# Optimization experiments

Hardware: AMD Instinct MI355X
Metric: run time of the kernel (lower is better)

The kernel has to match this reference:

```python
import jax, jax.numpy as jnp
import numpy as np

N = 50000      # n_nodes
E = 800000     # edges (before self-loops)
IN = 128       # in_dim
HID = 32       # hidden_dim (per-head out channels)
HEADS = 4
EMB = 128      # embed_dim
LAYERS = 3
NEG_SLOPE = 0.2  # PyG GATv2 default leaky_relu slope


def _layer_norm(x, g, b):
    mu = jnp.mean(x, axis=-1, keepdims=True)
    var = jnp.var(x, axis=-1, keepdims=True)
    return g * (x - mu) / jnp.sqrt(var + 1e-5) + b


def _gatv2(h, src, dst, n, Wl, bl, Wr, br, att, bias):
    # GATv2Conv (PyG semantics, share_weights=False, concat=True).
    H, C = att.shape
    xl = (h @ Wl + bl).reshape(n, H, C)   # target (i) transform
    xr = (h @ Wr + br).reshape(n, H, C)   # source (j) transform
    x_i = xl[dst]                          # [Etot, H, C] gather
    x_j = xr[src]
    e = jax.nn.leaky_relu(x_i + x_j, NEG_SLOPE)
    logit = jnp.einsum('ehc,hc->eh', e, att)          # [Etot, H]
    # segment softmax over destination node (every node has a self-loop)
    m = jax.ops.segment_max(logit, dst, num_segments=n)
    ex = jnp.exp(logit - m[dst])
    den = jax.ops.segment_sum(ex, dst, num_segments=n)
    alpha = ex / (den[dst] + 1e-16)
    out = jax.ops.segment_sum(alpha[..., None] * x_j, dst, num_segments=n)
    return out.reshape(n, H * C) + bias


def setup_inputs() -> dict:
    key = jax.random.key(0)
    ks = iter(jax.random.split(key, 64))
    d = {}
    d['x'] = jax.random.normal(next(ks), (N, IN), jnp.float32)
    d['edge_index'] = jax.random.randint(next(ks), (2, E), 0, N, dtype=jnp.int64)

    def w(shape, fan):
        return jax.random.normal(next(ks), shape, jnp.float32) / np.float32(np.sqrt(fan))

    HC = HID * HEADS
    d['W_in'] = w((IN, HID), IN); d['b_in'] = jnp.zeros((HID,), jnp.float32)
    for i in range(LAYERS):
        ic = HID if i == 0 else HC
        d[f'Wl{i}'] = w((ic, HC), ic); d[f'bl{i}'] = jnp.zeros((HC,), jnp.float32)
        d[f'Wr{i}'] = w((ic, HC), ic); d[f'br{i}'] = jnp.zeros((HC,), jnp.float32)
        d[f'att{i}'] = w((HEADS, HID), HID)
        d[f'bo{i}'] = jnp.zeros((HC,), jnp.float32)
        d[f'g{i}'] = jnp.ones((HC,), jnp.float32)
        d[f'be{i}'] = jnp.zeros((HC,), jnp.float32)
    d['W_out'] = w((HC, EMB), HC); d['b_out'] = jnp.zeros((EMB,), jnp.float32)
    return d


def reference(x, edge_index, W_in, b_in,
              Wl0, bl0, Wr0, br0, att0, bo0, g0, be0,
              Wl1, bl1, Wr1, br1, att1, bo1, g1, be1,
              Wl2, bl2, Wr2, br2, att2, bo2, g2, be2,
              W_out, b_out):
    n = x.shape[0]
    loops = jnp.arange(n, dtype=edge_index.dtype)  # add_self_loops=True
    src = jnp.concatenate([edge_index[0], loops])
    dst = jnp.concatenate([edge_index[1], loops])

    h = jax.nn.gelu(x @ W_in + b_in, approximate=False)
    layers = [(Wl0, bl0, Wr0, br0, att0, bo0, g0, be0),
              (Wl1, bl1, Wr1, br1, att1, bo1, g1, be1),
              (Wl2, bl2, Wr2, br2, att2, bo2, g2, be2)]
    for (Wl, bl, Wr, br, att, bo, g, be) in layers:
        h_new = jax.nn.gelu(_layer_norm(_gatv2(h, src, dst, n, Wl, bl, Wr, br, att, bo), g, be), approximate=False)
        h = h + h_new if h.shape == h_new.shape else h_new  # dropout = identity (eval)
    out = h @ W_out + b_out
    norm = jnp.maximum(jnp.linalg.norm(out, axis=-1, keepdims=True), 1e-12)
    return out / norm
```

## Files before the change

### kernel.cpp

```cpp
#include <hip/hip_runtime.h>
#include <hip/hip_bf16.h>
#include <math.h>

#define N_NODES 50000
#define N_EDGES 800000
#define IN_DIM  128
#define HC_DIM  128
#define HID_C   32
#define SCAN_NB 196

typedef __attribute__((ext_vector_type(8))) short short8;
typedef __attribute__((ext_vector_type(4))) float f32x4;

__device__ __forceinline__ float gelu_f(float x){
    return 0.5f*x*(1.0f + erff(x*0.7071067811865475f));
}

__device__ __forceinline__ void split2(float f, short& h, short& l){
    __hip_bfloat16 bh = __float2bfloat16(f);
    float r = f - __bfloat162float(bh);
    __hip_bfloat16 blo = __float2bfloat16(r);
    h = *reinterpret_cast<short*>(&bh);
    l = *reinterpret_cast<short*>(&blo);
}

__global__ __launch_bounds__(256) void k_zero(int* __restrict__ p, int n){
    int i = blockIdx.x*256 + threadIdx.x;
    if(i<n) p[i]=0;
}

__global__ __launch_bounds__(256) void k_count(const int* __restrict__ dst, int* __restrict__ cnt){
    int e = blockIdx.x*256 + threadIdx.x;
    if(e<N_EDGES) atomicAdd(&cnt[dst[e]], 1);
}

__global__ __launch_bounds__(256) void k_scan1(const int* __restrict__ cnt, int* __restrict__ rowptr,
                                               int* __restrict__ part){
    __shared__ int sh[256];
    int t=threadIdx.x; int i=blockIdx.x*256+t;
    int v = (i<N_NODES)? cnt[i] : 0;
    sh[t]=v; __syncthreads();
    for(int off=1; off<256; off<<=1){
        int y = (t>=off)? sh[t-off] : 0;
        __syncthreads();
        sh[t] += y;
        __syncthreads();
    }
    if(i<N_NODES) rowptr[i] = sh[t]-v;
    if(t==255) part[blockIdx.x] = sh[255];
}

__global__ __launch_bounds__(256) void k_scan2(int* __restrict__ part){
    __shared__ int sh[256];
    int t=threadIdx.x;
    int v = (t<SCAN_NB)? part[t] : 0;
    sh[t]=v; __syncthreads();
    for(int off=1; off<256; off<<=1){
        int y=(t>=off)? sh[t-off]:0;
        __syncthreads();
        sh[t]+=y;
        __syncthreads();
    }
    if(t<SCAN_NB) part[t] = sh[t]-v;
}

__global__ __launch_bounds__(256) void k_scan3(int* __restrict__ rowptr, const int* __restrict__ part,
                                               int* __restrict__ cur){
    int t=threadIdx.x; int i=blockIdx.x*256+t;
    if(i<N_NODES){
        int v = rowptr[i] + part[blockIdx.x];
        rowptr[i]=v; cur[i]=v;
    }
    if(i==0) rowptr[N_NODES]=N_EDGES;
}

__global__ __launch_bounds__(256) void k_fill(const int* __restrict__ src, const int* __restrict__ dst,
                                              int* __restrict__ cur, int* __restrict__ col){
    int e = blockIdx.x*256+threadIdx.x;
    if(e<N_EDGES){
        int d = dst[e];
        int p = atomicAdd(&cur[d],1);
        col[p] = src[e];
    }
}

__global__ __launch_bounds__(256) void k_gemm_in(const float* __restrict__ x, const float* __restrict__ W,
                                                 const float* __restrict__ b, float* __restrict__ h){
    int id = blockIdx.x*256+threadIdx.x;
    int r = id>>5, c = id&31;
    const float4* x4 = (const float4*)(x + (size_t)r*IN_DIM);
    float acc=0.f;
    #pragma unroll 8
    for(int k=0;k<IN_DIM/4;k++){
        float4 xv = x4[k];
        acc = fmaf(xv.x, W[(4*k  )*HID_C+c], acc);
        acc = fmaf(xv.y, W[(4*k+1)*HID_C+c], acc);
        acc = fmaf(xv.z, W[(4*k+2)*HID_C+c], acc);
        acc = fmaf(xv.w, W[(4*k+3)*HID_C+c], acc);
    }
    h[r*HID_C+c] = gelu_f(acc + b[c]);
}

template<int K, bool PAIR>
__global__ __launch_bounds__(256) void k_mfma(const float* __restrict__ A,
                                              const float* __restrict__ Wl, const float* __restrict__ bl,
                                              const float* __restrict__ Wr, const float* __restrict__ br,
                                              float* __restrict__ XL, float* __restrict__ XR){
    constexpr int KC  = 32;
    constexpr int LDS_K = KC + 8;
    constexpr int NCH = K / KC;
    __shared__ short As_hi[64*LDS_K], As_lo[64*LDS_K];
    __shared__ short Wlh[64*LDS_K],  Wll[64*LDS_K];
    __shared__ short Wrh[64*LDS_K],  Wrl[64*LDS_K];

    int t = threadIdx.x;
    int lane = t & 63, wave = t >> 6;
    int quad = lane >> 4, ml = lane & 15;
    int rbase = blockIdx.x * 64;
    int nbase = blockIdx.y * 64;

    f32x4 accL[4], accR[4];
    #pragma unroll
    for(int i=0;i<4;i++){ accL[i] = (f32x4){0.f,0.f,0.f,0.f}; accR[i] = (f32x4){0.f,0.f,0.f,0.f}; }

    for(int c=0; c<NCH; c++){
        if(c) __syncthreads();
        {
            int r = t >> 2, seg = t & 3;
            int gr = rbase + r; if(gr >= N_NODES) gr = N_NODES-1;
            const float* src = A + (size_t)gr*K + c*KC + seg*8;
            float4 f0 = *(const float4*)src;
            float4 f1 = *(const float4*)(src+4);
            float fs[8] = {f0.x,f0.y,f0.z,f0.w,f1.x,f1.y,f1.z,f1.w};
            short8 vh, vl;
            #pragma unroll
            for(int j=0;j<8;j++){ short h,l; split2(fs[j],h,l); vh[j]=h; vl[j]=l; }
            *(short8*)(As_hi + r*LDS_K + seg*8) = vh;
            *(short8*)(As_lo + r*LDS_K + seg*8) = vl;
        }
        {
            int n = t & 63, kq = t >> 6;
            #pragma unroll
            for(int p=0;p<8;p++){
                int kl = kq + p*4;
                short h,l;
                split2(Wl[(size_t)(c*KC + kl)*HC_DIM + nbase + n], h, l);
                Wlh[n*LDS_K + kl] = h; Wll[n*LDS_K + kl] = l;
                if(PAIR){
                    split2(Wr[(size_t)(c*KC + kl)*HC_DIM + nbase + n], h, l);
                    Wrh[n*LDS_K + kl] = h; Wrl[n*LDS_K + kl] = l;
                }
            }
        }
        __syncthreads();
        int k0 = quad*8;
        short8 wlh = *(const short8*)(Wlh + (wave*16 + ml)*LDS_K + k0);
        short8 wll = *(const short8*)(Wll + (wave*16 + ml)*LDS_K + k0);
        short8 wrh, wrl;
        if(PAIR){
            wrh = *(const short8*)(Wrh + (wave*16 + ml)*LDS_K + k0);
            wrl = *(const short8*)(Wrl + (wave*16 + ml)*LDS_K + k0);
        }
        #pragma unroll
        for(int i=0;i<4;i++){
            short8 ah = *(const short8*)(As_hi + (16*i + ml)*LDS_K + k0);
            short8 al = *(const short8*)(As_lo + (16*i + ml)*LDS_K + k0);
            accL[i] = __builtin_amdgcn_mfma_f32_16x16x32_bf16(ah, wlh, accL[i], 0,0,0);
            accL[i] = __builtin_amdgcn_mfma_f32_16x16x32_bf16(ah, wll, accL[i], 0,0,0);
            accL[i] = __builtin_amdgcn_mfma_f32_16x16x32_bf16(al, wlh, accL[i], 0,0,0);
            if(PAIR){
                accR[i] = __builtin_amdgcn_mfma_f32_16x16x32_bf16(ah, wrh, accR[i], 0,0,0);
                accR[i] = __builtin_amdgcn_mfma_f32_16x16x32_bf16(ah, wrl, accR[i], 0,0,0);
                accR[i] = __builtin_amdgcn_mfma_f32_16x16x32_bf16(al, wrh, accR[i], 0,0,0);
            }
        }
    }

    int col = nbase + wave*16 + ml;
    float bL = bl[col];
    float bR = PAIR ? br[col] : 0.f;
    #pragma unroll
    for(int i=0;i<4;i++){
        int row0 = rbase + 16*i + quad*4;
        #pragma unroll
        for(int r=0;r<4;r++){
            int gr = row0 + r;
            if(gr < N_NODES){
                XL[(size_t)gr*HC_DIM + col] = accL[i][r] + bL;
                if(PAIR) XR[(size_t)gr*HC_DIM + col] = accR[i][r] + bR;
            }
        }
    }
}

__global__ __launch_bounds__(256) void k_rownorm(const float* __restrict__ tmp, float* __restrict__ out){
    int wave=threadIdx.x>>6, lane=threadIdx.x&63;
    int node = blockIdx.x*4+wave;
    float2 v = *(const float2*)(tmp + (size_t)node*HC_DIM + 2*lane);
    float ss = v.x*v.x + v.y*v.y;
    #pragma unroll
    for(int msk=1;msk<64;msk<<=1) ss += __shfl_xor(ss,msk);
    float inv = 1.0f / fmaxf(sqrtf(ss), 1e-12f);
    *(float2*)(out + (size_t)node*HC_DIM + 2*lane) = make_float2(v.x*inv, v.y*inv);
}

__global__ __launch_bounds__(256) void k_node(const float* __restrict__ XL, const float* __restrict__ XR,
    const int* __restrict__ rowptr, const int* __restrict__ colidx,
    const float* __restrict__ att, const float* __restrict__ bo,
    const float* __restrict__ gg, const float* __restrict__ be,
    const float* __restrict__ hold, float* __restrict__ hout)
{
    int wave=threadIdx.x>>6, lane=threadIdx.x&63;
    int node = blockIdx.x*4+wave;
    int cg = lane & 31, half = lane >> 5;
    int c4 = cg << 2;

    float4 xl = *(const float4*)(XL + (size_t)node*HC_DIM + c4);
    float4 av = *(const float4*)(att + c4);
    int beg = rowptr[node], end = rowptr[node+1];

    #define EDGE_LOGIT(xj, q) { \
        float u0 = xl.x + xj.x; u0 = (u0>0.f)?u0:0.2f*u0; \
        float u1 = xl.y + xj.y; u1 = (u1>0.f)?u1:0.2f*u1; \
        float u2 = xl.z + xj.z; u2 = (u2>0.f)?u2:0.2f*u2; \
        float u3 = xl.w + xj.w; u3 = (u3>0.f)?u3:0.2f*u3; \
        q = fmaf(u0,av.x, fmaf(u1,av.y, fmaf(u2,av.z, u3*av.w))); \
        q += __shfl_xor(q,1); q += __shfl_xor(q,2); q += __shfl_xor(q,4); }

    float4 xs = *(const float4*)(XR + (size_t)node*HC_DIM + c4);
    float qs; EDGE_LOGIT(xs, qs)
    float m, ls; float4 acc;
    if(half==0){ m = qs; ls = 1.f; acc = xs; }
    else       { m = -INFINITY; ls = 0.f; acc = make_float4(0.f,0.f,0.f,0.f); }

    int P = end - beg;
    int nb = P >> 3;
    int base = beg;
    for(int b=0; b<nb; b++, base += 8){
        int j0 = colidx[base     + half];
        int j1 = colidx[base + 2 + half];
        int j2 = colidx[base + 4 + half];
        int j3 = colidx[base + 6 + half];
        float4 x0 = *(const float4*)(XR + (size_t)j0*HC_DIM + c4);
        float4 x1 = *(const float4*)(XR + (size_t)j1*HC_DIM + c4);
        float4 x2 = *(const float4*)(XR + (size_t)j2*HC_DIM + c4);
        float4 x3 = *(const float4*)(XR + (size_t)j3*HC_DIM + c4);
        float q0,q1,q2,q3;
        EDGE_LOGIT(x0,q0) EDGE_LOGIT(x1,q1) EDGE_LOGIT(x2,q2) EDGE_LOGIT(x3,q3)
        float nm = fmaxf(m, fmaxf(fmaxf(q0,q1),fmaxf(q2,q3)));
        float sc = __expf(m-nm);
        float e0 = __expf(q0-nm), e1 = __expf(q1-nm);
        float e2 = __expf(q2-nm), e3 = __expf(q3-nm);
        ls = fmaf(ls, sc, (e0+e1)+(e2+e3));
        acc.x = fmaf(acc.x, sc, fmaf(e0,x0.x, fmaf(e1,x1.x, fmaf(e2,x2.x, e3*x3.x))));
        acc.y = fmaf(acc.y, sc, fmaf(e0,x0.y, fmaf(e1,x1.y, fmaf(e2,x2.y, e3*x3.y))));
        acc.z = fmaf(acc.z, sc, fmaf(e0,x0.z, fmaf(e1,x1.z, fmaf(e2,x2.z, e3*x3.z))));
        acc.w = fmaf(acc.w, sc, fmaf(e0,x0.w, fmaf(e1,x1.w, fmaf(e2,x2.w, e3*x3.w))));
        m = nm;
    }
    #pragma unroll
    for(int i=0;i<4;i++){
        int idx = base + 2*i + half;
        if(idx < end){
            int j = colidx[idx];
            float4 xj = *(const float4*)(XR + (size_t)j*HC_DIM + c4);
            float q; EDGE_LOGIT(xj, q)
            float nm = fmaxf(m, q);
            float sc = __expf(m-nm);
            float p  = __expf(q-nm);
            ls = fmaf(ls, sc, p);
            acc.x = fmaf(acc.x, sc, p*xj.x);
            acc.y = fmaf(acc.y, sc, p*xj.y);
            acc.z = fmaf(acc.z, sc, p*xj.z);
            acc.w = fmaf(acc.w, sc, p*xj.w);
            m = nm;
        }
    }
    #undef EDGE_LOGIT

    {
        float mo  = __shfl_xor(m, 32);
        float lso = __shfl_xor(ls, 32);
        float4 ao;
        ao.x = __shfl_xor(acc.x,32); ao.y = __shfl_xor(acc.y,32);
        ao.z = __shfl_xor(acc.z,32); ao.w = __shfl_xor(acc.w,32);
        float nm = fmaxf(m, mo);
        float s0 = __expf(m-nm), s1 = __expf(mo-nm);
        ls = ls*s0 + lso*s1;
        acc.x = acc.x*s0 + ao.x*s1;
        acc.y = acc.y*s0 + ao.y*s1;
        acc.z = acc.z*s0 + ao.z*s1;
        acc.w = acc.w*s0 + ao.w*s1;
    }

    float inv = 1.0f/ls;
    float4 bo4 = *(const float4*)(bo + c4);
    float o0 = fmaf(acc.x,inv,bo4.x), o1 = fmaf(acc.y,inv,bo4.y);
    float o2 = fmaf(acc.z,inv,bo4.z), o3 = fmaf(acc.w,inv,bo4.w);
    float s1v = (o0+o1)+(o2+o3);
    float s2v = fmaf(o0,o0, fmaf(o1,o1, fmaf(o2,o2, o3*o3)));
    #pragma unroll
    for(int msk=1;msk<32;msk<<=1){ s1v += __shfl_xor(s1v,msk); s2v += __shfl_xor(s2v,msk); }
    float mean = s1v*(1.f/128.f);
    float var  = s2v*(1.f/128.f) - mean*mean;
    float rstd = rsqrtf(var + 1e-5f);
    float4 g4  = *(const float4*)(gg + c4);
    float4 be4 = *(const float4*)(be + c4);
    float r0 = gelu_f(fmaf(g4.x*(o0-mean), rstd, be4.x));
    float r1 = gelu_f(fmaf(g4.y*(o1-mean), rstd, be4.y));
    float r2 = gelu_f(fmaf(g4.z*(o2-mean), rstd, be4.z));
    float r3 = gelu_f(fmaf(g4.w*(o3-mean), rstd, be4.w));
    if(hold){
        float4 hv = *(const float4*)(hold + (size_t)node*HC_DIM + c4);
        r0 += hv.x; r1 += hv.y; r2 += hv.z; r3 += hv.w;
    }
    if(half==0)
        *(float4*)(hout + (size_t)node*HC_DIM + c4) = make_float4(r0,r1,r2,r3);
}

extern "C" void kernel_launch(void* const* d_in, const int* in_sizes, int n_in,
                              void* d_out, int out_size, void* d_ws, size_t ws_size,
                              hipStream_t stream)
{
    const float* x   = (const float*)d_in[0];
    const int*   ei  = (const int*)  d_in[1];
    const float* Win = (const float*)d_in[2];
    const float* bin = (const float*)d_in[3];
    const float *Wl[3], *bl[3], *Wr[3], *br[3], *att[3], *bo[3], *gg[3], *be[3];
    for(int i=0;i<3;i++){
        const int base = 4 + 8*i;
        Wl[i]=(const float*)d_in[base+0]; bl[i]=(const float*)d_in[base+1];
        Wr[i]=(const float*)d_in[base+2]; br[i]=(const float*)d_in[base+3];
        att[i]=(const float*)d_in[base+4]; bo[i]=(const float*)d_in[base+5];
        gg[i]=(const float*)d_in[base+6]; be[i]=(const float*)d_in[base+7];
    }
    const float* Wout=(const float*)d_in[28];
    const float* bout=(const float*)d_in[29];
    float* out = (float*)d_out;

    char* w = (char*)d_ws;
    float* hA = (float*)w;  w += (size_t)N_NODES*HC_DIM*4;
    float* hB = (float*)w;  w += (size_t)N_NODES*HC_DIM*4;
    float* XL = (float*)w;  w += (size_t)N_NODES*HC_DIM*4;
    float* XR = (float*)w;  w += (size_t)N_NODES*HC_DIM*4;
    int* rowptr = (int*)w;  w += (size_t)(N_NODES+2)*4;
    int* cursor = (int*)w;  w += (size_t)N_NODES*4;
    int* colidx = (int*)w;  w += (size_t)N_EDGES*4;
    int* part   = (int*)w;  w += 256*4;

    const int* srcp = ei;
    const int* dstp = ei + N_EDGES;

    const dim3 gemm_grid(782, 2);

    k_zero  <<<196, 256, 0, stream>>>(cursor, N_NODES);
    k_count <<<3125,256, 0, stream>>>(dstp, cursor);
    k_scan1 <<<SCAN_NB,256,0,stream>>>(cursor, rowptr, part);
    k_scan2 <<<1,   256, 0, stream>>>(part);
    k_scan3 <<<SCAN_NB,256,0,stream>>>(rowptr, part, cursor);
    k_fill  <<<3125,256, 0, stream>>>(srcp, dstp, cursor, colidx);

    k_gemm_in<<<6250,256,0,stream>>>(x, Win, bin, hA);

    k_mfma<32,true><<<gemm_grid,256,0,stream>>>(hA, Wl[0], bl[0], Wr[0], br[0], XL, XR);
    k_node<<<12500,256,0,stream>>>(XL,XR,rowptr,colidx,att[0],bo[0],gg[0],be[0], (const float*)nullptr, hB);

    k_mfma<128,true><<<gemm_grid,256,0,stream>>>(hB, Wl[1], bl[1], Wr[1], br[1], XL, XR);
    k_node<<<12500,256,0,stream>>>(XL,XR,rowptr,colidx,att[1],bo[1],gg[1],be[1], hB, hA);

    k_mfma<128,true><<<gemm_grid,256,0,stream>>>(hA, Wl[2], bl[2], Wr[2], br[2], XL, XR);
    k_node<<<12500,256,0,stream>>>(XL,XR,rowptr,colidx,att[2],bo[2],gg[2],be[2], hA, hB);

    k_mfma<128,false><<<gemm_grid,256,0,stream>>>(hB, Wout, bout, nullptr, nullptr, XL, nullptr);
    k_rownorm<<<12500,256,0,stream>>>(XL, out);
}
```

Measured before the change: 563.8 us.

## Pre-split weights and activations into bf16 hi/lo planes outside the GEMM

```diff
diff --git a/kernel.cpp b/kernel.cpp
--- a/kernel.cpp
+++ b/kernel.cpp
@@ -10,6 +10,7 @@
 #define SCAN_NB 196
 
 typedef __attribute__((ext_vector_type(8))) short short8;
+typedef __attribute__((ext_vector_type(4))) short short4v;
 typedef __attribute__((ext_vector_type(4))) float f32x4;
 
 __device__ __forceinline__ float gelu_f(float x){
@@ -22,11 +23,6 @@
     __hip_bfloat16 blo = __float2bfloat16(r);
     h = *reinterpret_cast<short*>(&bh);
     l = *reinterpret_cast<short*>(&blo);
-}
-
-__global__ __launch_bounds__(256) void k_zero(int* __restrict__ p, int n){
-    int i = blockIdx.x*256 + threadIdx.x;
-    if(i<n) p[i]=0;
 }
 
 __global__ __launch_bounds__(256) void k_count(const int* __restrict__ dst, int* __restrict__ cnt){
@@ -84,8 +80,41 @@
     }
 }
 
+__global__ __launch_bounds__(256) void k_splitW(const float* __restrict__ W0, const float* __restrict__ W1,
+                                                const float* __restrict__ W2, const float* __restrict__ W3,
+                                                const float* __restrict__ W4, const float* __restrict__ W5,
+                                                const float* __restrict__ W6, short* __restrict__ WT){
+    int bx = blockIdx.x;
+    int m, kc;
+    if(bx < 2){ m = bx; kc = 0; }
+    else { m = 2 + (bx-2)/4; kc = (bx-2)&3; }
+    const float* src; int K; size_t off;
+    switch(m){
+        case 0: src=W0; K=32;  off=0;      break;
+        case 1: src=W1; K=32;  off=8192;   break;
+        case 2: src=W2; K=128; off=16384;  break;
+        case 3: src=W3; K=128; off=49152;  break;
+        case 4: src=W4; K=128; off=81920;  break;
+        case 5: src=W5; K=128; off=114688; break;
+        default:src=W6; K=128; off=147456; break;
+    }
+    short* hi = WT + off;
+    short* lo = hi + (size_t)K*HC_DIM;
+    #pragma unroll
+    for(int i=0;i<16;i++){
+        int idx = threadIdx.x + i*256;
+        int k = kc*32 + (idx>>7);
+        int n = idx & 127;
+        float f = src[(size_t)k*HC_DIM + n];
+        short h,l; split2(f,h,l);
+        hi[(size_t)n*K + k] = h;
+        lo[(size_t)n*K + k] = l;
+    }
+}
+
 __global__ __launch_bounds__(256) void k_gemm_in(const float* __restrict__ x, const float* __restrict__ W,
-                                                 const float* __restrict__ b, float* __restrict__ h){
+                                                 const float* __restrict__ b, float* __restrict__ h,
+                                                 short* __restrict__ hhi, short* __restrict__ hlo){
     int id = blockIdx.x*256+threadIdx.x;
     int r = id>>5, c = id&31;
     const float4* x4 = (const float4*)(x + (size_t)r*IN_DIM);
@@ -98,13 +127,17 @@
         acc = fmaf(xv.z, W[(4*k+2)*HID_C+c], acc);
         acc = fmaf(xv.w, W[(4*k+3)*HID_C+c], acc);
     }
-    h[r*HID_C+c] = gelu_f(acc + b[c]);
+    float v = gelu_f(acc + b[c]);
+    h[(size_t)r*HID_C+c] = v;
+    short hh,ll; split2(v,hh,ll);
+    hhi[(size_t)r*HID_C+c] = hh;
+    hlo[(size_t)r*HID_C+c] = ll;
 }
 
 template<int K, bool PAIR>
-__global__ __launch_bounds__(256) void k_mfma(const float* __restrict__ A,
-                                              const float* __restrict__ Wl, const float* __restrict__ bl,
-                                              const float* __restrict__ Wr, const float* __restrict__ br,
+__global__ __launch_bounds__(256) void k_mfma(const short* __restrict__ Ahi, const short* __restrict__ Alo,
+                                              const short* __restrict__ WTl, const float* __restrict__ bl,
+                                              const short* __restrict__ WTr, const float* __restrict__ br,
                                               float* __restrict__ XL, float* __restrict__ XR){
     constexpr int KC  = 32;
     constexpr int LDS_K = KC + 8;
@@ -119,40 +152,30 @@
     int rbase = blockIdx.x * 64;
     int nbase = blockIdx.y * 64;
 
+    const short* WTl_lo = WTl + (size_t)K*HC_DIM;
+    const short* WTr_lo = PAIR ? (WTr + (size_t)K*HC_DIM) : nullptr;
+
     f32x4 accL[4], accR[4];
     #pragma unroll
     for(int i=0;i<4;i++){ accL[i] = (f32x4){0.f,0.f,0.f,0.f}; accR[i] = (f32x4){0.f,0.f,0.f,0.f}; }
+
+    int r = t >> 2, seg = t & 3;
+    int gr = rbase + r; if(gr >= N_NODES) gr = N_NODES-1;
 
     for(int c=0; c<NCH; c++){
         if(c) __syncthreads();
-        {
-            int r = t >> 2, seg = t & 3;
-            int gr = rbase + r; if(gr >= N_NODES) gr = N_NODES-1;
-            const float* src = A + (size_t)gr*K + c*KC + seg*8;
-            float4 f0 = *(const float4*)src;
-            float4 f1 = *(const float4*)(src+4);
-            float fs[8] = {f0.x,f0.y,f0.z,f0.w,f1.x,f1.y,f1.z,f1.w};
-            short8 vh, vl;
-            #pragma unroll
-            for(int j=0;j<8;j++){ short h,l; split2(fs[j],h,l); vh[j]=h; vl[j]=l; }
-            *(short8*)(As_hi + r*LDS_K + seg*8) = vh;
-            *(short8*)(As_lo + r*LDS_K + seg*8) = vl;
-        }
-        {
-            int n = t & 63, kq = t >> 6;
-            #pragma unroll
-            for(int p=0;p<8;p++){
-                int kl = kq + p*4;
-                short h,l;
-                split2(Wl[(size_t)(c*KC + kl)*HC_DIM + nbase + n], h, l);
-                Wlh[n*LDS_K + kl] = h; Wll[n*LDS_K + kl] = l;
-                if(PAIR){
-                    split2(Wr[(size_t)(c*KC + kl)*HC_DIM + nbase + n], h, l);
-                    Wrh[n*LDS_K + kl] = h; Wrl[n*LDS_K + kl] = l;
-                }
-            }
+        size_t ka = (size_t)gr*K + c*KC + seg*8;
+        *(short8*)(As_hi + r*LDS_K + seg*8) = *(const short8*)(Ahi + ka);
+        *(short8*)(As_lo + r*LDS_K + seg*8) = *(const short8*)(Alo + ka);
+        size_t kw = (size_t)(nbase + r)*K + c*KC + seg*8;
+        *(short8*)(Wlh + r*LDS_K + seg*8) = *(const short8*)(WTl + kw);
+        *(short8*)(Wll + r*LDS_K + seg*8) = *(const short8*)(WTl_lo + kw);
+        if(PAIR){
+            *(short8*)(Wrh + r*LDS_K + seg*8) = *(const short8*)(WTr + kw);
+            *(short8*)(Wrl + r*LDS_K + seg*8) = *(const short8*)(WTr_lo + kw);
         }
         __syncthreads();
+
         int k0 = quad*8;
         short8 wlh = *(const short8*)(Wlh + (wave*16 + ml)*LDS_K + k0);
         short8 wll = *(const short8*)(Wll + (wave*16 + ml)*LDS_K + k0);
@@ -183,11 +206,11 @@
     for(int i=0;i<4;i++){
         int row0 = rbase + 16*i + quad*4;
         #pragma unroll
-        for(int r=0;r<4;r++){
-            int gr = row0 + r;
-            if(gr < N_NODES){
-                XL[(size_t)gr*HC_DIM + col] = accL[i][r] + bL;
-                if(PAIR) XR[(size_t)gr*HC_DIM + col] = accR[i][r] + bR;
+        for(int rr=0;rr<4;rr++){
+            int grr = row0 + rr;
+            if(grr < N_NODES){
+                XL[(size_t)grr*HC_DIM + col] = accL[i][rr] + bL;
+                if(PAIR) XR[(size_t)grr*HC_DIM + col] = accR[i][rr] + bR;
             }
         }
     }
@@ -208,7 +231,8 @@
     const int* __restrict__ rowptr, const int* __restrict__ colidx,
     const float* __restrict__ att, const float* __restrict__ bo,
     const float* __restrict__ gg, const float* __restrict__ be,
-    const float* __restrict__ hold, float* __restrict__ hout)
+    const float* __restrict__ hold, float* __restrict__ hout,
+    short* __restrict__ hi_out, short* __restrict__ lo_out)
 {
     int wave=threadIdx.x>>6, lane=threadIdx.x&63;
     int node = blockIdx.x*4+wave;
@@ -314,8 +338,16 @@
         float4 hv = *(const float4*)(hold + (size_t)node*HC_DIM + c4);
         r0 += hv.x; r1 += hv.y; r2 += hv.z; r3 += hv.w;
     }
-    if(half==0)
+    if(half==0){
         *(float4*)(hout + (size_t)node*HC_DIM + c4) = make_float4(r0,r1,r2,r3);
+        short4v vh, vl; short hh, ll;
+        split2(r0,hh,ll); vh[0]=hh; vl[0]=ll;
+        split2(r1,hh,ll); vh[1]=hh; vl[1]=ll;
+        split2(r2,hh,ll); vh[2]=hh; vl[2]=ll;
+        split2(r3,hh,ll); vh[3]=hh; vl[3]=ll;
+        *(short4v*)(hi_out + (size_t)node*HC_DIM + c4) = vh;
+        *(short4v*)(lo_out + (size_t)node*HC_DIM + c4) = vl;
+    }
 }
 
 extern "C" void kernel_launch(void* const* d_in, const int* in_sizes, int n_in,
@@ -343,6 +375,11 @@
     float* hB = (float*)w;  w += (size_t)N_NODES*HC_DIM*4;
     float* XL = (float*)w;  w += (size_t)N_NODES*HC_DIM*4;
     float* XR = (float*)w;  w += (size_t)N_NODES*HC_DIM*4;
+    short* hAhi = (short*)w; w += (size_t)N_NODES*HC_DIM*2;
+    short* hAlo = (short*)w; w += (size_t)N_NODES*HC_DIM*2;
+    short* hBhi = (short*)w; w += (size_t)N_NODES*HC_DIM*2;
+    short* hBlo = (short*)w; w += (size_t)N_NODES*HC_DIM*2;
+    short* WT   = (short*)w; w += (size_t)180224*2;
     int* rowptr = (int*)w;  w += (size_t)(N_NODES+2)*4;
     int* cursor = (int*)w;  w += (size_t)N_NODES*4;
     int* colidx = (int*)w;  w += (size_t)N_EDGES*4;
@@ -353,24 +390,31 @@
 
     const dim3 gemm_grid(782, 2);
 
-    k_zero  <<<196, 256, 0, stream>>>(cursor, N_NODES);
+    k_splitW<<<22,256,0,stream>>>(Wl[0],Wr[0],Wl[1],Wr[1],Wl[2],Wr[2],Wout, WT);
+    const short* WTl0 = WT + 0;      const short* WTr0 = WT + 8192;
+    const short* WTl1 = WT + 16384;  const short* WTr1 = WT + 49152;
+    const short* WTl2 = WT + 81920;  const short* WTr2 = WT + 114688;
+    const short* WTo  = WT + 147456;
+
+    hipMemsetAsync(cursor, 0, (size_t)N_NODES*4, stream);
     k_count <<<3125,256, 0, stream>>>(dstp, cursor);
     k_scan1 <<<SCAN_NB,256,0,stream>>>(cursor, rowptr, part);
     k_scan2 <<<1,   256, 0, stream>>>(part);
     k_scan3 <<<SCAN_NB,256,0,stream>>>(rowptr, part, cursor);
     k_fill  <<<3125,256, 0, stream>>>(srcp, dstp, cursor, colidx);
 
-    k_gemm_in<<<6250,256,0,stream>>>(x, Win, bin, hA);
-
-    k_mfma<32,true><<<gemm_grid,256,0,stream>>>(hA, Wl[0], bl[0], Wr[0], br[0], XL, XR);
-    k_node<<<12500,256,0,stream>>>(XL,XR,rowptr,colidx,att[0],bo[0],gg[0],be[0], (const float*)nullptr, hB);
-
-    k_mfma<128,true><<<gemm_grid,256,0,stream>>>(hB, Wl[1], bl[1], Wr[1], br[1], XL, XR);
-    k_node<<<12500,256,0,stream>>>(XL,XR,rowptr,colidx,att[1],bo[1],gg[1],be[1], hB, hA);
-
-    k_mfma<128,true><<<gemm_grid,256,0,stream>>>(hA, Wl[2], bl[2], Wr[2], br[2], XL, XR);
-    k_node<<<12500,256,0,stream>>>(XL,XR,rowptr,colidx,att[2],bo[2],gg[2],be[2], hA, hB);
-
-    k_mfma<128,false><<<gemm_grid,256,0,stream>>>(hB, Wout, bout, nullptr, nullptr, XL, nullptr);
+    k_gemm_in<<<6250,256,0,stream>>>(x, Win, bin, hA, hAhi, hAlo);
+
+    k_mfma<32,true><<<gemm_grid,256,0,stream>>>(hAhi, hAlo, WTl0, bl[0], WTr0, br[0], XL, XR);
+    k_node<<<12500,256,0,stream>>>(XL,XR,rowptr,colidx,att[0],bo[0],gg[0],be[0],
+                                   (const float*)nullptr, hB, hBhi, hBlo);
+
+    k_mfma<128,true><<<gemm_grid,256,0,stream>>>(hBhi, hBlo, WTl1, bl[1], WTr1, br[1], XL, XR);
+    k_node<<<12500,256,0,stream>>>(XL,XR,rowptr,colidx,att[1],bo[1],gg[1],be[1], hB, hA, hAhi, hAlo);
+
+    k_mfma<128,true><<<gemm_grid,256,0,stream>>>(hAhi, hAlo, WTl2, bl[2], WTr2, br[2], XL, XR);
+    k_node<<<12500,256,0,stream>>>(XL,XR,rowptr,colidx,att[2],bo[2],gg[2],be[2], hA, hB, hBhi, hBlo);
+
+    k_mfma<128,false><<<gemm_grid,256,0,stream>>>(hBhi, hBlo, WTo, bout, nullptr, nullptr, XL, nullptr);
     k_rownorm<<<12500,256,0,stream>>>(XL, out);
 }
```

After: 572.4 us. No clear change (+1.5%).
